# Performance work log

Hardware: AMD Instinct MI355X
Metric: run time of the kernel (lower is better)

## Reference

```python
import jax, jax.numpy as jnp
import numpy as np

B, N, C, G = 32, 1024, 64, 64

def setup_inputs() -> dict:
    key = jax.random.key(0)
    ks = jax.random.split(key, 8)
    return {
        "x": jax.random.normal(ks[0], (B, N, C), dtype=jnp.float32),
        "valid_len": jax.random.randint(ks[1], (B,), 0, N, dtype=jnp.int64) if jax.config.jax_enable_x64 else jax.random.randint(ks[1], (B,), 0, N, dtype=jnp.int32),
        "Wq": jax.random.normal(ks[2], (C, G), dtype=jnp.float32) * 0.1,
        "bq": jax.random.normal(ks[3], (G,), dtype=jnp.float32) * 0.1,
        "Wk": jax.random.normal(ks[4], (C, G), dtype=jnp.float32) * 0.1,
        "bk": jax.random.normal(ks[5], (G,), dtype=jnp.float32) * 0.1,
        "Wv": jax.random.normal(ks[6], (C, G), dtype=jnp.float32) * 0.1,
        "bv": jax.random.normal(ks[7], (G,), dtype=jnp.float32) * 0.1,
    }

def reference(x, valid_len, Wq, bq, Wk, bk, Wv, bv):
    # x: [B, N, C]; valid_len: [B] int (number of valid key positions per batch)
    q = x @ Wq + bq                                   # [B, N, G]
    k = x @ Wk + bk                                   # [B, N, G]
    v = x @ Wv + bv                                   # [B, N, G]
    scores = jnp.einsum('bnd,bmd->bnm', q, k)         # [B, N, N] (no 1/sqrt(d) scale)
    # mask: key positions >= valid_len[b] get -1e6 (matches original's -1000000.0 fill)
    col = jnp.arange(scores.shape[-1])
    mask = col[None, None, :] >= valid_len[:, None, None]
    scores = jnp.where(mask, jnp.float32(-1000000.0), scores)
    attn = jax.nn.softmax(scores, axis=-1)            # [B, N, N]
    return jnp.einsum('bnm,bmd->bnd', attn, v)        # [B, N, G]
```

## Files before the change

kernel.cpp:

```cpp
#include <hip/hip_runtime.h>
#include <stdint.h>


typedef __attribute__((ext_vector_type(4))) float    floatx4;
typedef __attribute__((ext_vector_type(8))) _Float16 halfx8;

static __device__ __forceinline__ unsigned short f2h(float f) {
    union { _Float16 h; unsigned short u; } v; v.h = (_Float16)f;
    return v.u;
}
static __device__ __forceinline__ float h2f(unsigned short u) {
    union { unsigned short u; _Float16 h; } v; v.u = u;
    return (float)v.h;
}

__global__ __launch_bounds__(256) void wprep_kernel(
    const float* __restrict__ Wq, const float* __restrict__ Wk,
    const float* __restrict__ Wv, unsigned short* __restrict__ wt_pack)
{
    const int plane = blockIdx.x;
    const int wi = plane >> 1, hl = plane & 1;
    const float* W = (wi == 0) ? Wq : (wi == 1) ? Wk : Wv;
    const int tid = threadIdx.x;
    const int g = tid & 63, cb = (tid >> 6) * 16;
#pragma unroll
    for (int j = 0; j < 16; ++j) {
        int c = cb + j;
        float f = W[c * 64 + g];
        unsigned short hi = f2h(f);
        unsigned short v = hl ? f2h(f - h2f(hi)) : hi;
        int idx = g * 64 + ((((c >> 3) ^ (g & 7))) * 8) + (c & 7);
        wt_pack[plane * 4096 + idx] = v;
    }
}

__global__ __launch_bounds__(256) void qkv_proj_kernel(
    const float* __restrict__ x,
    const unsigned short* __restrict__ wt_pack,
    const float* __restrict__ bq, const float* __restrict__ bk, const float* __restrict__ bv,
    unsigned short* __restrict__ q_ws, unsigned short* __restrict__ k_ws,
    unsigned short* __restrict__ vt_ws)
{
    __shared__ __align__(16) unsigned short smem[8 * 4096];
    float* vtmp = (float*)&smem[2 * 4096];

    const int XS_HI = 0, XS_LO = 4096;
    #define WT_OFF(i) (2 * 4096 + (i) * 4096)

    const int tid  = threadIdx.x;
    const int blk  = blockIdx.x;
    const int row0 = blk * 64;
    const int b    = blk >> 4;
    const int n0   = (blk & 15) * 64;
    const int lane = tid & 63;
    const int w    = tid >> 6;
    const int l15  = lane & 15;
    const int quad = lane >> 4;

#pragma unroll
    for (int i = 0; i < 6; ++i) {
#pragma unroll
        for (int pp = 0; pp < 2; ++pp) {
            int e = (pp * 256 + tid) * 8;
            *(uint4*)&smem[2 * 4096 + i * 4096 + e] =
                *(const uint4*)&wt_pack[i * 4096 + e];
        }
    }

#pragma unroll
    for (int i = 0; i < 2; ++i) {
        int id = i * 256 + tid;
        int r = id >> 3, c8 = id & 7;
        const float4* gp = (const float4*)(x + (row0 + r) * 64 + c8 * 8);
        float4 f0 = gp[0], f1 = gp[1];
        float fv[8] = { f0.x, f0.y, f0.z, f0.w, f1.x, f1.y, f1.z, f1.w };
        __align__(16) unsigned short thi[8], tlo[8];
#pragma unroll
        for (int j = 0; j < 8; ++j) {
            unsigned short hi = f2h(fv[j]);
            thi[j] = hi;
            tlo[j] = f2h(fv[j] - h2f(hi));
        }
        int idx = r * 64 + ((c8 ^ (r & 7)) * 8);
        *(uint4*)&smem[XS_HI + idx] = *(uint4*)thi;
        *(uint4*)&smem[XS_LO + idx] = *(uint4*)tlo;
    }
    __syncthreads();

    const int arow = w * 16 + l15;
    const int aidx0 = arow * 64 + (((0 + quad) ^ (arow & 7)) * 8);
    const int aidx1 = arow * 64 + (((4 + quad) ^ (arow & 7)) * 8);
    halfx8 a_hi0 = *(const halfx8*)&smem[XS_HI + aidx0];
    halfx8 a_hi1 = *(const halfx8*)&smem[XS_HI + aidx1];
    halfx8 a_lo0 = *(const halfx8*)&smem[XS_LO + aidx0];
    halfx8 a_lo1 = *(const halfx8*)&smem[XS_LO + aidx1];

    __syncthreads();

    unsigned short* q_lds = &smem[0];
    unsigned short* k_lds = &smem[4096];

    const float* biases[3] = { bq, bk, bv };
    floatx4 vacc[4];
#pragma unroll
    for (int wi = 0; wi < 3; ++wi) {
#pragma unroll
        for (int gs = 0; gs < 4; ++gs) {
            int g0 = gs * 16;
            float bias = biases[wi][g0 + l15];
            floatx4 acc = { bias, bias, bias, bias };
            int brow = g0 + l15;
            int bidx0 = brow * 64 + (((0 + quad) ^ (brow & 7)) * 8);
            int bidx1 = brow * 64 + (((4 + quad) ^ (brow & 7)) * 8);
            halfx8 b_hi0 = *(const halfx8*)&smem[WT_OFF(wi * 2 + 0) + bidx0];
            halfx8 b_hi1 = *(const halfx8*)&smem[WT_OFF(wi * 2 + 0) + bidx1];
            halfx8 b_lo0 = *(const halfx8*)&smem[WT_OFF(wi * 2 + 1) + bidx0];
            halfx8 b_lo1 = *(const halfx8*)&smem[WT_OFF(wi * 2 + 1) + bidx1];
            acc = __builtin_amdgcn_mfma_f32_16x16x32_f16(a_hi0, b_hi0, acc, 0, 0, 0);
            acc = __builtin_amdgcn_mfma_f32_16x16x32_f16(a_hi1, b_hi1, acc, 0, 0, 0);
            acc = __builtin_amdgcn_mfma_f32_16x16x32_f16(a_hi0, b_lo0, acc, 0, 0, 0);
            acc = __builtin_amdgcn_mfma_f32_16x16x32_f16(a_hi1, b_lo1, acc, 0, 0, 0);
            acc = __builtin_amdgcn_mfma_f32_16x16x32_f16(a_lo0, b_hi0, acc, 0, 0, 0);
            acc = __builtin_amdgcn_mfma_f32_16x16x32_f16(a_lo1, b_hi1, acc, 0, 0, 0);
            if (wi < 2) {
                unsigned short* dst = (wi == 0) ? q_lds : k_lds;
                int c8 = gs * 2 + (l15 >> 3);
#pragma unroll
                for (int r = 0; r < 4; ++r) {
                    int row = w * 16 + quad * 4 + r;
                    dst[row * 64 + ((c8 ^ (row & 7)) * 8) + (l15 & 7)] = f2h(acc[r]);
                }
            } else {
                vacc[gs] = acc;
            }
        }
    }

    __syncthreads();

#pragma unroll
    for (int i = 0; i < 2; ++i) {
        int id = i * 256 + tid;
        int r = id >> 3, c8 = id & 7;
        int sidx = r * 64 + ((c8 ^ (r & 7)) * 8);
        *(uint4*)(q_ws + (row0 + r) * 64 + c8 * 8) = *(const uint4*)&q_lds[sidx];
        *(uint4*)(k_ws + (row0 + r) * 64 + c8 * 8) = *(const uint4*)&k_lds[sidx];
    }

#pragma unroll
    for (int gs = 0; gs < 4; ++gs) {
#pragma unroll
        for (int r = 0; r < 4; ++r) {
            int nl = w * 16 + quad * 4 + r;
            vtmp[(gs * 16 + l15) * 65 + nl] = vacc[gs][r];
        }
    }
    __syncthreads();
    {
        int g = tid >> 2, c4 = tid & 3;
        __align__(16) unsigned short tmp[16];
#pragma unroll
        for (int j = 0; j < 16; ++j) tmp[j] = f2h(vtmp[g * 65 + c4 * 16 + j]);
        unsigned short* dst = vt_ws + (b * 64 + g) * 1024 + n0 + c4 * 16;
        *(uint4*)(dst)     = ((uint4*)tmp)[0];
        *(uint4*)(dst + 8) = ((uint4*)tmp)[1];
    }
    #undef WT_OFF
}

__global__ __launch_bounds__(256) void attn_kernel(
    const unsigned short* __restrict__ q_ws, const unsigned short* __restrict__ k_ws,
    const unsigned short* __restrict__ vt_ws, const int* __restrict__ valid_len,
    float* __restrict__ out)
{
    __shared__ __align__(16) unsigned short qs[4096];
    __shared__ __align__(16) unsigned short kbuf[2][4096];
    __shared__ __align__(16) unsigned short vbuf[2][4096];
    __shared__ __align__(16) unsigned short ps[4 * 1024];

    const int tid  = threadIdx.x;
    const int blk  = blockIdx.x;
    const int b    = blk >> 4;
    const int row0 = blk * 64;
    const int lane = tid & 63;
    const int w    = tid >> 6;
    const int l15  = lane & 15;
    const int quad = lane >> 4;

    const int r_a  = tid >> 3,          c8_a = tid & 7;
    const int r_b  = (256 + tid) >> 3,  c8_b = tid & 7;
    const int lidx_a = r_a * 64 + ((c8_a ^ (r_a & 7)) * 8);
    const int lidx_b = r_b * 64 + ((c8_b ^ (r_b & 7)) * 8);

    *(uint4*)&qs[lidx_a] = *(const uint4*)(q_ws + (row0 + r_a) * 64 + c8_a * 8);
    *(uint4*)&qs[lidx_b] = *(const uint4*)(q_ws + (row0 + r_b) * 64 + c8_b * 8);

    const int vl    = valid_len[b];
    const int nt    = (vl == 0) ? 16 : ((vl + 63) >> 6);
    const int fullt = vl >> 6;

    const unsigned short* kbase = k_ws + (size_t)b * 1024 * 64;
    const unsigned short* vbase = vt_ws + (size_t)b * 64 * 1024;

    uint4 kr0 = *(const uint4*)(kbase + r_a * 64 + c8_a * 8);
    uint4 kr1 = *(const uint4*)(kbase + r_b * 64 + c8_b * 8);
    uint4 vr0 = *(const uint4*)(vbase + r_a * 1024 + c8_a * 8);
    uint4 vr1 = *(const uint4*)(vbase + r_b * 1024 + c8_b * 8);
    *(uint4*)&kbuf[0][lidx_a] = kr0;
    *(uint4*)&kbuf[0][lidx_b] = kr1;
    *(uint4*)&vbuf[0][lidx_a] = vr0;
    *(uint4*)&vbuf[0][lidx_b] = vr1;

    __syncthreads();

    const int arow = w * 16 + l15;
    halfx8 aq0 = *(const halfx8*)&qs[arow * 64 + (((0 + quad) ^ (arow & 7)) * 8)];
    halfx8 aq1 = *(const halfx8*)&qs[arow * 64 + (((4 + quad) ^ (arow & 7)) * 8)];

    float m_r[4]    = { -INFINITY, -INFINITY, -INFINITY, -INFINITY };
    float l_lane[4] = { 0.f, 0.f, 0.f, 0.f };
    floatx4 o[4] = { {0,0,0,0}, {0,0,0,0}, {0,0,0,0}, {0,0,0,0} };

    for (int t = 0; t < nt; ++t) {
        bool pre = (t + 1) < nt;
        if (pre) {
            const unsigned short* kp = kbase + (t + 1) * 64 * 64;
            const unsigned short* vp = vbase + (t + 1) * 64;
            kr0 = *(const uint4*)(kp + r_a * 64 + c8_a * 8);
            kr1 = *(const uint4*)(kp + r_b * 64 + c8_b * 8);
            vr0 = *(const uint4*)(vp + r_a * 1024 + c8_a * 8);
            vr1 = *(const uint4*)(vp + r_b * 1024 + c8_b * 8);
        }
        if (t > 0) __syncthreads();
        if (pre) {
            *(uint4*)&kbuf[(t + 1) & 1][lidx_a] = kr0;
            *(uint4*)&kbuf[(t + 1) & 1][lidx_b] = kr1;
            *(uint4*)&vbuf[(t + 1) & 1][lidx_a] = vr0;
            *(uint4*)&vbuf[(t + 1) & 1][lidx_b] = vr1;
        }
        const unsigned short* ksb = kbuf[t & 1];
        const unsigned short* vsb = vbuf[t & 1];

        floatx4 s[4];
#pragma unroll
        for (int sub = 0; sub < 4; ++sub) {
            int krow = sub * 16 + l15;
            halfx8 bk0 = *(const halfx8*)&ksb[krow * 64 + (((0 + quad) ^ (krow & 7)) * 8)];
            halfx8 bk1 = *(const halfx8*)&ksb[krow * 64 + (((4 + quad) ^ (krow & 7)) * 8)];
            floatx4 acc = { 0, 0, 0, 0 };
            acc = __builtin_amdgcn_mfma_f32_16x16x32_f16(aq0, bk0, acc, 0, 0, 0);
            acc = __builtin_amdgcn_mfma_f32_16x16x32_f16(aq1, bk1, acc, 0, 0, 0);
            s[sub] = acc;
        }
        if (t >= fullt) {
#pragma unroll
            for (int sub = 0; sub < 4; ++sub) {
                int key = t * 64 + sub * 16 + l15;
                if (key >= vl) { s[sub][0] = -1e6f; s[sub][1] = -1e6f; s[sub][2] = -1e6f; s[sub][3] = -1e6f; }
            }
        }

        float p[4][4];
        float alpha[4];
#pragma unroll
        for (int r = 0; r < 4; ++r) {
            float mx = fmaxf(fmaxf(s[0][r], s[1][r]), fmaxf(s[2][r], s[3][r]));
#pragma unroll
            for (int off = 1; off < 16; off <<= 1)
                mx = fmaxf(mx, __shfl_xor(mx, off, 64));
            float mnew = fmaxf(m_r[r], mx);
            alpha[r] = __expf(m_r[r] - mnew);
            float psum = 0.f;
#pragma unroll
            for (int sub = 0; sub < 4; ++sub) {
                float pv = __expf(s[sub][r] - mnew);
                p[sub][r] = pv;
                psum += pv;
            }
            l_lane[r] = l_lane[r] * alpha[r] + psum;
            m_r[r] = mnew;
        }
#pragma unroll
        for (int gs = 0; gs < 4; ++gs) {
            o[gs][0] *= alpha[0]; o[gs][1] *= alpha[1];
            o[gs][2] *= alpha[2]; o[gs][3] *= alpha[3];
        }

        unsigned short* psw = &ps[w * 1024];
#pragma unroll
        for (int sub = 0; sub < 4; ++sub) {
            int c8 = sub * 2 + (l15 >> 3);
#pragma unroll
            for (int r = 0; r < 4; ++r) {
                int row = quad * 4 + r;
                psw[row * 64 + ((c8 ^ (row & 7)) * 8) + (l15 & 7)] = f2h(p[sub][r]);
            }
        }
        halfx8 ap0 = *(const halfx8*)&psw[l15 * 64 + (((0 + quad) ^ (l15 & 7)) * 8)];
        halfx8 ap1 = *(const halfx8*)&psw[l15 * 64 + (((4 + quad) ^ (l15 & 7)) * 8)];

#pragma unroll
        for (int gs = 0; gs < 4; ++gs) {
            int grow = gs * 16 + l15;
            halfx8 bv0 = *(const halfx8*)&vsb[grow * 64 + (((0 + quad) ^ (grow & 7)) * 8)];
            halfx8 bv1 = *(const halfx8*)&vsb[grow * 64 + (((4 + quad) ^ (grow & 7)) * 8)];
            o[gs] = __builtin_amdgcn_mfma_f32_16x16x32_f16(ap0, bv0, o[gs], 0, 0, 0);
            o[gs] = __builtin_amdgcn_mfma_f32_16x16x32_f16(ap1, bv1, o[gs], 0, 0, 0);
        }
    }

    float l[4];
#pragma unroll
    for (int r = 0; r < 4; ++r) {
        float ss = l_lane[r];
#pragma unroll
        for (int off = 1; off < 16; off <<= 1)
            ss += __shfl_xor(ss, off, 64);
        l[r] = ss;
    }
#pragma unroll
    for (int gs = 0; gs < 4; ++gs) {
#pragma unroll
        for (int r = 0; r < 4; ++r) {
            int row = row0 + w * 16 + quad * 4 + r;
            out[row * 64 + gs * 16 + l15] = o[gs][r] / l[r];
        }
    }
}

extern "C" void kernel_launch(void* const* d_in, const int* in_sizes, int n_in,
                              void* d_out, int out_size, void* d_ws, size_t ws_size,
                              hipStream_t stream) {
    const float* x    = (const float*)d_in[0];
    const int*   vlen = (const int*)  d_in[1];
    const float* Wq   = (const float*)d_in[2];
    const float* bq   = (const float*)d_in[3];
    const float* Wk   = (const float*)d_in[4];
    const float* bk   = (const float*)d_in[5];
    const float* Wv   = (const float*)d_in[6];
    const float* bv   = (const float*)d_in[7];
    float* out = (float*)d_out;

    unsigned short* q_ws    = (unsigned short*)d_ws;
    unsigned short* k_ws    = q_ws + 32768 * 64;
    unsigned short* vt_ws   = k_ws + 32768 * 64;
    unsigned short* wt_pack = vt_ws + 32 * 64 * 1024;

    wprep_kernel<<<6, 256, 0, stream>>>(Wq, Wk, Wv, wt_pack);
    qkv_proj_kernel<<<512, 256, 0, stream>>>(x, wt_pack, bq, bk, bv, q_ws, k_ws, vt_ws);
    attn_kernel<<<512, 256, 0, stream>>>(q_ws, k_ws, vt_ws, vlen, out);
}
```

Measured before the change: 107.8 us.

## Fuse weight prep, QKV projection and attention into one kernel with grid barrier

Merges the three launches into one persistent kernel. Each block converts the weights to split fp16 in LDS itself, keeps its Q tile in shared memory instead of writing it to global, and waits at a global atomic-counter grid barrier before the attention phase reads K/V. This removes two kernel launches and the Q round trip through memory. In exchange it adds a memset launch and a spin barrier whose correctness depends on all 512 blocks being co-resident (launch bounds 256,2). It also repeats the weight conversion in every block.

```diff
diff --git a/kernel.cpp b/kernel.cpp
--- a/kernel.cpp
+++ b/kernel.cpp
@@ -14,32 +14,14 @@
     return (float)v.h;
 }
 
-__global__ __launch_bounds__(256) void wprep_kernel(
-    const float* __restrict__ Wq, const float* __restrict__ Wk,
-    const float* __restrict__ Wv, unsigned short* __restrict__ wt_pack)
-{
-    const int plane = blockIdx.x;
-    const int wi = plane >> 1, hl = plane & 1;
-    const float* W = (wi == 0) ? Wq : (wi == 1) ? Wk : Wv;
-    const int tid = threadIdx.x;
-    const int g = tid & 63, cb = (tid >> 6) * 16;
-#pragma unroll
-    for (int j = 0; j < 16; ++j) {
-        int c = cb + j;
-        float f = W[c * 64 + g];
-        unsigned short hi = f2h(f);
-        unsigned short v = hl ? f2h(f - h2f(hi)) : hi;
-        int idx = g * 64 + ((((c >> 3) ^ (g & 7))) * 8) + (c & 7);
-        wt_pack[plane * 4096 + idx] = v;
-    }
-}
-
-__global__ __launch_bounds__(256) void qkv_proj_kernel(
+__global__ __launch_bounds__(256, 2) void fused_attn_kernel(
     const float* __restrict__ x,
-    const unsigned short* __restrict__ wt_pack,
-    const float* __restrict__ bq, const float* __restrict__ bk, const float* __restrict__ bv,
-    unsigned short* __restrict__ q_ws, unsigned short* __restrict__ k_ws,
-    unsigned short* __restrict__ vt_ws)
+    const float* __restrict__ Wq, const float* __restrict__ bq,
+    const float* __restrict__ Wk, const float* __restrict__ bk,
+    const float* __restrict__ Wv, const float* __restrict__ bv,
+    const int* __restrict__ valid_len,
+    unsigned short* __restrict__ k_ws, unsigned short* __restrict__ vt_ws,
+    unsigned int* ctr, float* __restrict__ out)
 {
     __shared__ __align__(16) unsigned short smem[8 * 4096];
     float* vtmp = (float*)&smem[2 * 4096];
@@ -58,16 +40,6 @@
     const int quad = lane >> 4;
 
 #pragma unroll
-    for (int i = 0; i < 6; ++i) {
-#pragma unroll
-        for (int pp = 0; pp < 2; ++pp) {
-            int e = (pp * 256 + tid) * 8;
-            *(uint4*)&smem[2 * 4096 + i * 4096 + e] =
-                *(const uint4*)&wt_pack[i * 4096 + e];
-        }
-    }
-
-#pragma unroll
     for (int i = 0; i < 2; ++i) {
         int id = i * 256 + tid;
         int r = id >> 3, c8 = id & 7;
@@ -84,6 +56,23 @@
         int idx = r * 64 + ((c8 ^ (r & 7)) * 8);
         *(uint4*)&smem[XS_HI + idx] = *(uint4*)thi;
         *(uint4*)&smem[XS_LO + idx] = *(uint4*)tlo;
+    }
+    {
+        const float* Ws[3] = { Wq, Wk, Wv };
+        int g = tid & 63, ci = tid >> 6;
+#pragma unroll
+        for (int wi = 0; wi < 3; ++wi) {
+#pragma unroll
+            for (int j = 0; j < 16; ++j) {
+                int c = ci * 16 + j;
+                float f = Ws[wi][c * 64 + g];
+                unsigned short hi = f2h(f);
+                unsigned short lo = f2h(f - h2f(hi));
+                int idx = g * 64 + (((c >> 3) ^ (g & 7)) * 8) + (c & 7);
+                smem[WT_OFF(wi * 2 + 0) + idx] = hi;
+                smem[WT_OFF(wi * 2 + 1) + idx] = lo;
+            }
+        }
     }
     __syncthreads();
 
@@ -143,7 +132,6 @@
         int id = i * 256 + tid;
         int r = id >> 3, c8 = id & 7;
         int sidx = r * 64 + ((c8 ^ (r & 7)) * 8);
-        *(uint4*)(q_ws + (row0 + r) * 64 + c8 * 8) = *(const uint4*)&q_lds[sidx];
         *(uint4*)(k_ws + (row0 + r) * 64 + c8 * 8) = *(const uint4*)&k_lds[sidx];
     }
 
@@ -166,35 +154,29 @@
         *(uint4*)(dst + 8) = ((uint4*)tmp)[1];
     }
     #undef WT_OFF
-}
-
-__global__ __launch_bounds__(256) void attn_kernel(
-    const unsigned short* __restrict__ q_ws, const unsigned short* __restrict__ k_ws,
-    const unsigned short* __restrict__ vt_ws, const int* __restrict__ valid_len,
-    float* __restrict__ out)
-{
-    __shared__ __align__(16) unsigned short qs[4096];
-    __shared__ __align__(16) unsigned short kbuf[2][4096];
-    __shared__ __align__(16) unsigned short vbuf[2][4096];
-    __shared__ __align__(16) unsigned short ps[4 * 1024];
-
-    const int tid  = threadIdx.x;
-    const int blk  = blockIdx.x;
-    const int b    = blk >> 4;
-    const int row0 = blk * 64;
-    const int lane = tid & 63;
-    const int w    = tid >> 6;
-    const int l15  = lane & 15;
-    const int quad = lane >> 4;
+
+    __threadfence();
+    __syncthreads();
+    if (tid == 0) {
+        atomicAdd(ctr, 1u);
+        while (atomicAdd(ctr, 0u) < gridDim.x)
+            __builtin_amdgcn_s_sleep(2);
+    }
+    __syncthreads();
+    __threadfence();
+
+    unsigned short* qs    = &smem[0];
+    unsigned short* kbufA = &smem[4096];
+    unsigned short* kbufB = &smem[8192];
+    unsigned short* vbufA = &smem[12288];
+    unsigned short* vbufB = &smem[16384];
+    unsigned short* ps    = &smem[20480];
 
     const int r_a  = tid >> 3,          c8_a = tid & 7;
     const int r_b  = (256 + tid) >> 3,  c8_b = tid & 7;
     const int lidx_a = r_a * 64 + ((c8_a ^ (r_a & 7)) * 8);
     const int lidx_b = r_b * 64 + ((c8_b ^ (r_b & 7)) * 8);
 
-    *(uint4*)&qs[lidx_a] = *(const uint4*)(q_ws + (row0 + r_a) * 64 + c8_a * 8);
-    *(uint4*)&qs[lidx_b] = *(const uint4*)(q_ws + (row0 + r_b) * 64 + c8_b * 8);
-
     const int vl    = valid_len[b];
     const int nt    = (vl == 0) ? 16 : ((vl + 63) >> 6);
     const int fullt = vl >> 6;
@@ -206,14 +188,13 @@
     uint4 kr1 = *(const uint4*)(kbase + r_b * 64 + c8_b * 8);
     uint4 vr0 = *(const uint4*)(vbase + r_a * 1024 + c8_a * 8);
     uint4 vr1 = *(const uint4*)(vbase + r_b * 1024 + c8_b * 8);
-    *(uint4*)&kbuf[0][lidx_a] = kr0;
-    *(uint4*)&kbuf[0][lidx_b] = kr1;
-    *(uint4*)&vbuf[0][lidx_a] = vr0;
-    *(uint4*)&vbuf[0][lidx_b] = vr1;
-
-    __syncthreads();
-
-    const int arow = w * 16 + l15;
+    *(uint4*)&kbufA[lidx_a] = kr0;
+    *(uint4*)&kbufA[lidx_b] = kr1;
+    *(uint4*)&vbufA[lidx_a] = vr0;
+    *(uint4*)&vbufA[lidx_b] = vr1;
+
+    __syncthreads();
+
     halfx8 aq0 = *(const halfx8*)&qs[arow * 64 + (((0 + quad) ^ (arow & 7)) * 8)];
     halfx8 aq1 = *(const halfx8*)&qs[arow * 64 + (((4 + quad) ^ (arow & 7)) * 8)];
 
@@ -233,13 +214,15 @@
         }
         if (t > 0) __syncthreads();
         if (pre) {
-            *(uint4*)&kbuf[(t + 1) & 1][lidx_a] = kr0;
-            *(uint4*)&kbuf[(t + 1) & 1][lidx_b] = kr1;
-            *(uint4*)&vbuf[(t + 1) & 1][lidx_a] = vr0;
-            *(uint4*)&vbuf[(t + 1) & 1][lidx_b] = vr1;
-        }
-        const unsigned short* ksb = kbuf[t & 1];
-        const unsigned short* vsb = vbuf[t & 1];
+            unsigned short* kn = ((t + 1) & 1) ? kbufB : kbufA;
+            unsigned short* vn = ((t + 1) & 1) ? vbufB : vbufA;
+            *(uint4*)&kn[lidx_a] = kr0;
+            *(uint4*)&kn[lidx_b] = kr1;
+            *(uint4*)&vn[lidx_a] = vr0;
+            *(uint4*)&vn[lidx_b] = vr1;
+        }
+        const unsigned short* ksb = (t & 1) ? kbufB : kbufA;
+        const unsigned short* vsb = (t & 1) ? vbufB : vbufA;
 
         floatx4 s[4];
 #pragma unroll
@@ -341,12 +324,12 @@
     const float* bv   = (const float*)d_in[7];
     float* out = (float*)d_out;
 
-    unsigned short* q_ws    = (unsigned short*)d_ws;
-    unsigned short* k_ws    = q_ws + 32768 * 64;
-    unsigned short* vt_ws   = k_ws + 32768 * 64;
-    unsigned short* wt_pack = vt_ws + 32 * 64 * 1024;
-
-    wprep_kernel<<<6, 256, 0, stream>>>(Wq, Wk, Wv, wt_pack);
-    qkv_proj_kernel<<<512, 256, 0, stream>>>(x, wt_pack, bq, bk, bv, q_ws, k_ws, vt_ws);
-    attn_kernel<<<512, 256, 0, stream>>>(q_ws, k_ws, vt_ws, vlen, out);
+    unsigned short* k_ws  = (unsigned short*)d_ws;
+    unsigned short* vt_ws = k_ws + 32768 * 64;
+    unsigned int*   ctr   = (unsigned int*)((char*)d_ws +
+                              (size_t)2 * (32768 * 64 + 32 * 64 * 1024));
+
+    hipMemsetAsync(ctr, 0, sizeof(unsigned int), stream);
+    fused_attn_kernel<<<512, 256, 0, stream>>>(
+        x, Wq, bq, Wk, bk, Wv, bv, vlen, k_ws, vt_ws, ctr, out);
 }
```

After: 207.6 us. +92.6%, slower.
